# Performance work log

Hardware: AMD Instinct MI355X
Metric: run time of the kernel (lower is better)

Reference implementation:

```python
import jax, jax.numpy as jnp
import numpy as np
import math

B, N0 = 128, 128          # graphs, nodes per graph
EPG = 512                 # edges per graph
F_IN, EDGE_DIM = 64, 16
EMB, HEADS = 128, 4
HC = EMB * HEADS
L = 2                     # stacked layers (pooling every layer: top_k_every_n=1)
RATIO = 0.5
DENSE = 256


def setup_inputs():
    rng = np.random.default_rng(0)

    def U(fan_in, *shape):
        s = 1.0 / np.sqrt(fan_in)
        return jnp.asarray(rng.uniform(-s, s, shape), dtype=jnp.float32)

    x = jnp.asarray(rng.standard_normal((B * N0, F_IN)), dtype=jnp.float32)
    src = rng.integers(0, N0, (B, EPG))
    dst = rng.integers(0, N0, (B, EPG))
    off = (np.arange(B) * N0)[:, None]
    edge_index = jnp.asarray(np.stack([(src + off).reshape(-1), (dst + off).reshape(-1)]), dtype=jnp.int32)
    edge_attr = jnp.asarray(rng.standard_normal((B * EPG, EDGE_DIM)), dtype=jnp.float32)

    inp = dict(x=x, edge_index=edge_index, edge_attr=edge_attr)
    inp.update(
        c1_Wq=U(F_IN, F_IN, HC), c1_bq=U(F_IN, HC),
        c1_Wk=U(F_IN, F_IN, HC), c1_bk=U(F_IN, HC),
        c1_Wv=U(F_IN, F_IN, HC), c1_bv=U(F_IN, HC),
        c1_We=U(EDGE_DIM, EDGE_DIM, HC),
        c1_Ws=U(F_IN, F_IN, HC), c1_bs=U(F_IN, HC),
        c1_Wb=U(3 * HC, 3 * HC),
        t1_W=U(HC, HC, EMB), t1_b=U(HC, EMB),
        bn1_g=jnp.ones(EMB), bn1_b=jnp.zeros(EMB),
        cl_Wq=U(EMB, L, EMB, HC), cl_bq=U(EMB, L, HC),
        cl_Wk=U(EMB, L, EMB, HC), cl_bk=U(EMB, L, HC),
        cl_Wv=U(EMB, L, EMB, HC), cl_bv=U(EMB, L, HC),
        cl_We=U(EDGE_DIM, L, EDGE_DIM, HC),
        cl_Ws=U(EMB, L, EMB, HC), cl_bs=U(EMB, L, HC),
        cl_Wb=U(3 * HC, L, 3 * HC),
        tl_W=U(HC, L, HC, EMB), tl_b=U(HC, L, EMB),
        bnl_g=jnp.ones((L, EMB)), bnl_b=jnp.zeros((L, EMB)),
        pool_w=U(EMB, L, EMB),
        l1_W=U(2 * EMB, 2 * EMB, DENSE), l1_b=U(2 * EMB, DENSE),
        l2_W=U(DENSE, DENSE, DENSE // 2), l2_b=U(DENSE, DENSE // 2),
        l3_W=U(DENSE // 2, DENSE // 2, 1), l3_b=U(DENSE // 2, 1),
    )
    return inp


def _tconv(x, src, dst, emask, ea, Wq, bq, Wk, bk, Wv, bv, We, Ws, bs, Wb, n_nodes):
    # PyG TransformerConv, beta=True, concat=True, edge features added to key and value
    H, C = HEADS, EMB
    q = (x @ Wq + bq).reshape(-1, H, C)
    k = (x @ Wk + bk).reshape(-1, H, C)
    v = (x @ Wv + bv).reshape(-1, H, C)
    e = (ea @ We).reshape(-1, H, C)
    kj = k[src] + e
    alpha = (q[dst] * kj).sum(-1) * (1.0 / math.sqrt(C))  # [E, H]
    mx = jax.ops.segment_max(jnp.where(emask[:, None], alpha, -jnp.inf), dst, num_segments=n_nodes)
    mx = jnp.where(jnp.isfinite(mx), mx, 0.0)
    p = jnp.where(emask[:, None], jnp.exp(alpha - mx[dst]), 0.0)
    p = p / (jax.ops.segment_sum(p, dst, num_segments=n_nodes)[dst] + 1e-16)
    msg = v[src] + e
    out = jax.ops.segment_sum(p[:, :, None] * msg, dst, num_segments=n_nodes).reshape(-1, H * C)
    skip = x @ Ws + bs
    beta = jax.nn.sigmoid(jnp.concatenate([out, skip, out - skip], -1) @ Wb)[:, None]
    return beta * skip + (1.0 - beta) * out


def _bn(x, g, b):
    # BatchNorm1d, training-mode batch statistics (biased variance)
    m = x.mean(0)
    v = ((x - m) ** 2).mean(0)
    return g * (x - m) * jax.lax.rsqrt(v + 1e-5) + b


def _topk_pool(x, src, dst, emask, w, n):
    # TopKPooling: score = x.w/|w|, keep top ceil(ratio*n) per graph, scale by tanh(score)
    k = int(math.ceil(RATIO * n))
    s = (x @ w) / jnp.linalg.norm(w)          # [B*n]
    _, idx = jax.lax.top_k(s.reshape(B, n), k)
    idx = jnp.sort(idx, axis=1)
    gidx = (jnp.arange(B)[:, None] * n + idx).reshape(-1)
    x_new = x[gidx] * jnp.tanh(s[gidx])[:, None]
    kept = jnp.zeros(B * n, bool).at[gidx].set(True)
    new_id = (jnp.cumsum(kept) - 1).astype(jnp.int32)
    em = emask & kept[src] & kept[dst]
    src_n = jnp.where(em, new_id[src], 0)
    dst_n = jnp.where(em, new_id[dst], 0)
    return x_new, src_n, dst_n, em, k


def _forward(edge_index, x, edge_attr, c1_Wq, c1_bq, c1_Wk, c1_bk, c1_Wv, c1_bv, c1_We, c1_Ws, c1_bs, c1_Wb,
             t1_W, t1_b, bn1_g, bn1_b, cl_Wq, cl_bq, cl_Wk, cl_bk, cl_Wv, cl_bv, cl_We, cl_Ws, cl_bs, cl_Wb,
             tl_W, tl_b, bnl_g, bnl_b, pool_w, l1_W, l1_b, l2_W, l2_b, l3_W, l3_b):
    src, dst = edge_index[0], edge_index[1]
    emask = jnp.ones(src.shape[0], bool)
    n = N0
    x = _tconv(x, src, dst, emask, edge_attr, c1_Wq, c1_bq, c1_Wk, c1_bk, c1_Wv, c1_bv, c1_We, c1_Ws, c1_bs, c1_Wb, B * n)
    x = _bn(jax.nn.relu(x @ t1_W + t1_b), bn1_g, bn1_b)
    reps = []
    for i in range(L):
        x = _tconv(x, src, dst, emask, edge_attr, cl_Wq[i], cl_bq[i], cl_Wk[i], cl_bk[i], cl_Wv[i], cl_bv[i],
                   cl_We[i], cl_Ws[i], cl_bs[i], cl_Wb[i], B * n)
        x = _bn(jax.nn.relu(x @ tl_W[i] + tl_b[i]), bnl_g[i], bnl_b[i])
        x, src, dst, emask, n = _topk_pool(x, src, dst, emask, pool_w[i], n)
        xg = x.reshape(B, n, EMB)
        reps.append(jnp.concatenate([xg.max(1), xg.mean(1)], -1))  # gmp || gap
    h = reps[0]
    for r in reps[1:]:
        h = h + r
    h = jax.nn.relu(h @ l1_W + l1_b)  # dropout p=0.8 is identity at eval
    h = jax.nn.relu(h @ l2_W + l2_b)
    return h @ l3_W + l3_b            # [B, 1]


def reference(x, edge_index, edge_attr, c1_Wq, c1_bq, c1_Wk, c1_bk, c1_Wv, c1_bv, c1_We, c1_Ws, c1_bs, c1_Wb,
              t1_W, t1_b, bn1_g, bn1_b, cl_Wq, cl_bq, cl_Wk, cl_bk, cl_Wv, cl_bv, cl_We, cl_Ws, cl_bs, cl_Wb,
              tl_W, tl_b, bnl_g, bnl_b, pool_w, l1_W, l1_b, l2_W, l2_b, l3_W, l3_b):
    return _forward(edge_index, x, edge_attr, c1_Wq, c1_bq, c1_Wk, c1_bk, c1_Wv, c1_bv, c1_We, c1_Ws, c1_bs, c1_Wb,
                    t1_W, t1_b, bn1_g, bn1_b, cl_Wq, cl_bq, cl_Wk, cl_bk, cl_Wv, cl_bv, cl_We, cl_Ws, cl_bs, cl_Wb,
                    tl_W, tl_b, bnl_g, bnl_b, pool_w, l1_W, l1_b, l2_W, l2_b, l3_W, l3_b)
```

## Files before the change

kernel.cpp:

```cpp
#include <hip/hip_runtime.h>
#include <math.h>

#define E_TOT 65536
#define B_G   128
#define QLD   1664
#define NCOL  1792

typedef __attribute__((ext_vector_type(8))) short short8;
typedef __attribute__((ext_vector_type(4))) short short4v;
typedef __attribute__((ext_vector_type(4))) float float4v;

__device__ __forceinline__ unsigned short f2bf(float f) {
    unsigned int u = __float_as_uint(f);
    unsigned int r = u + 0x7FFFu + ((u >> 16) & 1u);
    return (unsigned short)(r >> 16);
}
__device__ __forceinline__ float bf2f(unsigned short h) {
    return __uint_as_float(((unsigned int)h) << 16);
}

__global__ void wsplit_k(const float* __restrict__ Wst, const float* __restrict__ Wq,
                         const float* __restrict__ Wk, const float* __restrict__ Wvt,
                         const float* __restrict__ Wu, const float* __restrict__ Wvz,
                         const float* __restrict__ ws_z,
                         int K, int kshift, unsigned short* __restrict__ Whi,
                         unsigned short* __restrict__ Wlo) {
    int idx = blockIdx.x * 256 + threadIdx.x;
    if (idx >= NCOL * K) return;
    int col = idx >> kshift, k = idx & (K - 1);
    float w;
    if (col < 128)       w = Wst[k * 128 + col];
    else if (col < 640)  w = Wq[(size_t)k * 512 + col - 128];
    else if (col < 1152) w = Wk[(size_t)k * 512 + col - 640];
    else if (col < 1664) w = Wvt[(size_t)k * 512 + col - 1152];
    else if (col < 1728) w = Wu[(size_t)k * 64 + col - 1664];
    else if (col < 1732) w = Wvz[(size_t)k * 4 + col - 1728];
    else if (col == 1732) w = ws_z[k];
    else                 w = 0.f;
    unsigned short h = f2bf(w);
    Whi[idx] = h;
    Wlo[idx] = f2bf(w - bf2f(h));
}

__global__ void xsplit_k(const float* __restrict__ X, int total4,
                         unsigned short* __restrict__ Xhi, unsigned short* __restrict__ Xlo) {
    int idx = blockIdx.x * 256 + threadIdx.x;
    if (idx >= total4) return;
    float4 f = ((const float4*)X)[idx];
    unsigned short h0 = f2bf(f.x), h1 = f2bf(f.y), h2 = f2bf(f.z), h3 = f2bf(f.w);
    short4v hv = {(short)h0, (short)h1, (short)h2, (short)h3};
    short4v lv = {(short)f2bf(f.x - bf2f(h0)), (short)f2bf(f.y - bf2f(h1)),
                  (short)f2bf(f.z - bf2f(h2)), (short)f2bf(f.w - bf2f(h3))};
    *(short4v*)(Xhi + (size_t)idx * 4) = hv;
    *(short4v*)(Xlo + (size_t)idx * 4) = lv;
}

__global__ void twt_k(const float* __restrict__ tW, float* __restrict__ tWT) {
    int idx = blockIdx.x * 256 + threadIdx.x;
    int m = idx & 127, c = idx >> 7;
    tWT[m * 512 + c] = tW[idx];
}

template <int KT>
__global__ __launch_bounds__(256) void qkvs_mfma(
        const unsigned short* __restrict__ Xhi, const unsigned short* __restrict__ Xlo,
        const unsigned short* __restrict__ Whi, const unsigned short* __restrict__ Wlo,
        const float* __restrict__ bq, const float* __restrict__ bk,
        const float* __restrict__ bvt, const float* __restrict__ bu,
        const float* __restrict__ bvz, const float* __restrict__ zb,
        float* __restrict__ out, float* __restrict__ UB, float* __restrict__ VZB,
        float* __restrict__ SZB, int nwg8) {
    constexpr int NKC = KT >> 5;
    constexpr int NCH = KT >> 6;
    __shared__ __align__(16) unsigned short bs[2 * 64 * 80];
    const int ldb = 80, loHalf = 64 * 80;
    int tid = threadIdx.x;
    int wave = tid >> 6, lane = tid & 63;
    int m = lane & 15, kg = lane >> 4;
    int hw = blockIdx.y * 28 + blockIdx.x;
    int lb = (hw & 7) * nwg8 + (hw >> 3);
    int n0 = (lb / 28) * 128 + wave * 32;
    int c0 = (lb % 28) * 64;

    short8 ahi[2][NKC], alo[2][NKC];
#pragma unroll
    for (int rt = 0; rt < 2; ++rt) {
        const unsigned short* xh = Xhi + (size_t)(n0 + rt * 16 + m) * KT + kg * 8;
        const unsigned short* xl = Xlo + (size_t)(n0 + rt * 16 + m) * KT + kg * 8;
#pragma unroll
        for (int kc = 0; kc < NKC; ++kc) {
            ahi[rt][kc] = *(const short8*)(xh + kc * 32);
            alo[rt][kc] = *(const short8*)(xl + kc * 32);
        }
    }

    float4v acc[2][4];
#pragma unroll
    for (int rt = 0; rt < 2; ++rt)
#pragma unroll
        for (int ct = 0; ct < 4; ++ct) acc[rt][ct] = (float4v){0.f, 0.f, 0.f, 0.f};

    short8 ph[2][2], pl[2][2];
#pragma unroll
    for (int it = 0; it < 2; ++it) {
        int i = tid + it * 256; int col = i >> 3, part = i & 7;
        ph[0][it] = *(const short8*)(Whi + (size_t)(c0 + col) * KT + part * 8);
        pl[0][it] = *(const short8*)(Wlo + (size_t)(c0 + col) * KT + part * 8);
    }

#pragma unroll
    for (int ch = 0; ch < NCH; ++ch) {
        if (ch) __syncthreads();
#pragma unroll
        for (int it = 0; it < 2; ++it) {
            int i = tid + it * 256; int col = i >> 3, part = i & 7;
            *(short8*)(bs + col * ldb + part * 8) = ph[ch & 1][it];
            *(short8*)(bs + loHalf + col * ldb + part * 8) = pl[ch & 1][it];
        }
        __syncthreads();
        if (ch + 1 < NCH) {
#pragma unroll
            for (int it = 0; it < 2; ++it) {
                int i = tid + it * 256; int col = i >> 3, part = i & 7;
                ph[(ch + 1) & 1][it] =
                    *(const short8*)(Whi + (size_t)(c0 + col) * KT + (ch + 1) * 64 + part * 8);
                pl[(ch + 1) & 1][it] =
                    *(const short8*)(Wlo + (size_t)(c0 + col) * KT + (ch + 1) * 64 + part * 8);
            }
        }
#pragma unroll
        for (int kc2 = 0; kc2 < 2; ++kc2) {
            const int kc = ch * 2 + kc2;
#pragma unroll
            for (int ct = 0; ct < 4; ++ct) {
                const unsigned short* bp = bs + (ct * 16 + m) * ldb + kg * 8 + kc2 * 32;
                short8 bhi = *(const short8*)(bp);
                short8 blo = *(const short8*)(bp + loHalf);
                acc[0][ct] = __builtin_amdgcn_mfma_f32_16x16x32_bf16(ahi[0][kc], bhi, acc[0][ct], 0, 0, 0);
                acc[0][ct] = __builtin_amdgcn_mfma_f32_16x16x32_bf16(alo[0][kc], bhi, acc[0][ct], 0, 0, 0);
                acc[0][ct] = __builtin_amdgcn_mfma_f32_16x16x32_bf16(ahi[0][kc], blo, acc[0][ct], 0, 0, 0);
                acc[1][ct] = __builtin_amdgcn_mfma_f32_16x16x32_bf16(ahi[1][kc], bhi, acc[1][ct], 0, 0, 0);
                acc[1][ct] = __builtin_amdgcn_mfma_f32_16x16x32_bf16(alo[1][kc], bhi, acc[1][ct], 0, 0, 0);
                acc[1][ct] = __builtin_amdgcn_mfma_f32_16x16x32_bf16(ahi[1][kc], blo, acc[1][ct], 0, 0, 0);
            }
        }
    }

#pragma unroll
    for (int ct = 0; ct < 4; ++ct) {
        int col = c0 + ct * 16 + m;
        if (col > 1732) continue;
        float bias;
        if (col < 128)       bias = 0.f;
        else if (col < 640)  bias = bq[col - 128];
        else if (col < 1152) bias = bk[col - 640];
        else if (col < 1664) bias = bvt[col - 1152];
        else if (col < 1728) bias = bu[col - 1664];
        else if (col < 1732) bias = bvz[col - 1728];
        else                 bias = zb[0];
#pragma unroll
        for (int rt = 0; rt < 2; ++rt) {
#pragma unroll
            for (int r = 0; r < 4; ++r) {
                int row = n0 + rt * 16 + kg * 4 + r;
                float v = acc[rt][ct][r] + bias;
                if (col < 1664)      out[(size_t)row * QLD + col] = v;
                else if (col < 1728) UB[(size_t)row * 64 + col - 1664] = v;
                else if (col < 1732) VZB[(size_t)row * 4 + col - 1728] = v;
                else                 SZB[row] = v;
            }
        }
    }
}

__global__ void prep_k(const float* __restrict__ Ws, const float* __restrict__ bs,
                       const float* __restrict__ tWT, const float* __restrict__ Wb,
                       const float* __restrict__ Wq, const float* __restrict__ bq,
                       const float* __restrict__ We,
                       const float* __restrict__ Wv, const float* __restrict__ bv, int Fin,
                       float* __restrict__ Wst, float* __restrict__ ws_z,
                       float* __restrict__ sbt, float* __restrict__ zb,
                       float* __restrict__ Wu, float* __restrict__ bu,
                       float* __restrict__ Wet, float* __restrict__ wez,
                       float* __restrict__ Wvt, float* __restrict__ bvt,
                       float* __restrict__ Wvz, float* __restrict__ bvz) {
    int w = (blockIdx.x * blockDim.x + threadIdx.x) >> 6;
    int lane = threadIdx.x & 63;
    int o1 = Fin * 128, o2 = o1 + Fin, o3 = o2 + 128, o4 = o3 + 1;
    int o5 = o4 + Fin * 64, o6 = o5 + 64, o7 = o6 + 8192, o8 = o7 + 64;
    int o9 = o8 + Fin * 512, o10 = o9 + 512, o11 = o10 + Fin * 4, total = o11 + 4;
    if (w >= total) return;
    float s = 0.f;
    if (w < o1) {
        int f = w >> 7, m = w & 127;
        for (int c = lane; c < 512; c += 64)
            s = fmaf(Ws[(size_t)f * 512 + c], tWT[(size_t)m * 512 + c], s);
    } else if (w < o2) {
        int f = w - o1;
        for (int c = lane; c < 512; c += 64)
            s = fmaf(Ws[(size_t)f * 512 + c], Wb[512 + c] - Wb[1024 + c], s);
    } else if (w < o3) {
        int m = w - o2;
        for (int c = lane; c < 512; c += 64)
            s = fmaf(bs[c], tWT[(size_t)m * 512 + c], s);
    } else if (w < o4) {
        for (int c = lane; c < 512; c += 64)
            s = fmaf(bs[c], Wb[512 + c] - Wb[1024 + c], s);
    } else if (w < o5) {
        int q = w - o4; int f = q >> 6; int j2 = q & 63;
        int j = j2 & 15; int cb = (j2 >> 4) * 128;
        s = Wq[(size_t)f * 512 + cb + lane] * We[j * 512 + cb + lane]
          + Wq[(size_t)f * 512 + cb + lane + 64] * We[j * 512 + cb + lane + 64];
    } else if (w < o6) {
        int j2 = w - o5; int j = j2 & 15; int cb = (j2 >> 4) * 128;
        s = bq[cb + lane] * We[j * 512 + cb + lane]
          + bq[cb + lane + 64] * We[j * 512 + cb + lane + 64];
    } else if (w < o7) {
        int q = w - o6; int j2 = q >> 7; int m = q & 127;
        int j = j2 & 15; int cb = (j2 >> 4) * 128;
        s = We[j * 512 + cb + lane] * tWT[(size_t)m * 512 + cb + lane]
          + We[j * 512 + cb + lane + 64] * tWT[(size_t)m * 512 + cb + lane + 64];
    } else if (w < o8) {
        int j2 = w - o7; int j = j2 & 15; int cb = (j2 >> 4) * 128;
        s = We[j * 512 + cb + lane] * (Wb[cb + lane] + Wb[1024 + cb + lane])
          + We[j * 512 + cb + lane + 64] * (Wb[cb + lane + 64] + Wb[1024 + cb + lane + 64]);
    } else if (w < o9) {
        int q = w - o8; int f = q >> 9; int j2 = q & 511;
        int cb = (j2 >> 7) * 128; int m = j2 & 127;
        s = Wv[(size_t)f * 512 + cb + lane] * tWT[(size_t)m * 512 + cb + lane]
          + Wv[(size_t)f * 512 + cb + lane + 64] * tWT[(size_t)m * 512 + cb + lane + 64];
    } else if (w < o10) {
        int j2 = w - o9; int cb = (j2 >> 7) * 128; int m = j2 & 127;
        s = bv[cb + lane] * tWT[(size_t)m * 512 + cb + lane]
          + bv[cb + lane + 64] * tWT[(size_t)m * 512 + cb + lane + 64];
    } else if (w < o11) {
        int q = w - o10; int f = q >> 2; int cb = (q & 3) * 128;
        s = Wv[(size_t)f * 512 + cb + lane] * (Wb[cb + lane] + Wb[1024 + cb + lane])
          + Wv[(size_t)f * 512 + cb + lane + 64] * (Wb[cb + lane + 64] + Wb[1024 + cb + lane + 64]);
    } else {
        int cb = (w - o11) * 128;
        s = bv[cb + lane] * (Wb[cb + lane] + Wb[1024 + cb + lane])
          + bv[cb + lane + 64] * (Wb[cb + lane + 64] + Wb[1024 + cb + lane + 64]);
    }
#pragma unroll
    for (int off = 32; off; off >>= 1) s += __shfl_xor(s, off, 64);
    if (lane == 0) {
        if (w < o1) Wst[w] = s;
        else if (w < o2) ws_z[w - o1] = s;
        else if (w < o3) sbt[w - o2] = s;
        else if (w < o4) zb[0] = s;
        else if (w < o5) Wu[w - o4] = s;
        else if (w < o6) bu[w - o5] = s;
        else if (w < o7) Wet[w - o6] = s;
        else if (w < o8) wez[w - o7] = s;
        else if (w < o9) Wvt[w - o8] = s;
        else if (w < o10) bvt[w - o9] = s;
        else if (w < o11) Wvz[w - o10] = s;
        else bvz[w - o11] = s;
    }
}

__global__ __launch_bounds__(128) void csr_graph_k(const int* __restrict__ src,
                                                   const int* __restrict__ dst,
                                                   int* __restrict__ row_start,
                                                   int* __restrict__ row_end,
                                                   int* __restrict__ colb,
                                                   int* __restrict__ eidb) {
    __shared__ int cnt[128], pref[128], cur[128];
    int g = blockIdx.x, t = threadIdx.x;
    cnt[t] = 0;
    __syncthreads();
    int e0 = g * 512, nb = g * 128;
    int dl[4], sl[4];
#pragma unroll
    for (int i = 0; i < 4; ++i) {
        int e = e0 + t + i * 128;
        dl[i] = dst[e] - nb;
        sl[i] = src[e];
        atomicAdd(&cnt[dl[i]], 1);
    }
    __syncthreads();
    pref[t] = cnt[t];
    __syncthreads();
    for (int st = 1; st < 128; st <<= 1) {
        int v = (t >= st) ? pref[t - st] : 0;
        __syncthreads();
        pref[t] += v;
        __syncthreads();
    }
    int ex = pref[t] - cnt[t];
    row_start[nb + t] = e0 + ex;
    row_end[nb + t]   = e0 + pref[t];
    cur[t] = ex;
    __syncthreads();
#pragma unroll
    for (int i = 0; i < 4; ++i) {
        int pos = atomicAdd(&cur[dl[i]], 1);
        colb[e0 + pos] = sl[i];
        eidb[e0 + pos] = e0 + t + i * 128;
    }
}

__global__ __launch_bounds__(256) void attn_combine_k(
        const float* __restrict__ QB, const float* __restrict__ UB,
        const float* __restrict__ VZB, const float* __restrict__ SZB,
        const int* __restrict__ row_start, const int* __restrict__ row_end,
        const int* __restrict__ colb, const int* __restrict__ eidb,
        const float* __restrict__ ea, const float* __restrict__ wez,
        const float* __restrict__ Wet, const float* __restrict__ sbt,
        const float* __restrict__ tb, float* __restrict__ xn, int nwg8) {
    __shared__ float shO[4][4][128];
    __shared__ float tsh[4][64];
    __shared__ float zsh[4][4];
    int tid = threadIdx.x;
    int head = tid >> 6, lane = tid & 63;
    int grp = lane >> 4, li = lane & 15;
    int bid = blockIdx.x;
    int lb = (bid & 7) * nwg8 + (bid >> 3);
    int node = lb * 4 + grp;

    float wezv = wez[head * 16 + li];
    const float* Qr = QB + (size_t)node * QLD + 128 + head * 128 + li * 8;
    float4 q0 = *(const float4*)Qr;
    float4 q1 = *(const float4*)(Qr + 4);
    float uu = UB[(size_t)node * 64 + head * 16 + li];
    int beg = row_start[node], end = row_end[node];

    float l = 0.f, t = 0.f, zac = 0.f;
    float4 a0 = {0.f, 0.f, 0.f, 0.f}, a1 = {0.f, 0.f, 0.f, 0.f};
    const float scale = 0.08838834764831845f;
    int j = beg;
    for (; j + 1 < end; j += 2) {
        int s1 = colb[j],     e1 = eidb[j];
        int s2 = colb[j + 1], e2 = eidb[j + 1];
        const float* K1 = QB + (size_t)s1 * QLD + 640 + head * 128 + li * 8;
        const float* V1 = QB + (size_t)s1 * QLD + 1152 + head * 128 + li * 8;
        const float* K2 = QB + (size_t)s2 * QLD + 640 + head * 128 + li * 8;
        const float* V2 = QB + (size_t)s2 * QLD + 1152 + head * 128 + li * 8;
        float4 k10 = *(const float4*)K1, k11 = *(const float4*)(K1 + 4);
        float4 v10 = *(const float4*)V1, v11 = *(const float4*)(V1 + 4);
        float4 k20 = *(const float4*)K2, k21 = *(const float4*)(K2 + 4);
// ... 258 lines not shown
                       const float* __restrict__ W3, const float* __restrict__ b3,
                       float* __restrict__ out) {
    __shared__ float h[256], a1[256], a2[128], red[256];
    int g = blockIdx.x, t = threadIdx.x;
    h[t] = rep0[g * 256 + t] + rep1[g * 256 + t];
    __syncthreads();
    float acc = b1[t];
    for (int i = 0; i < 256; ++i) acc = fmaf(h[i], W1[i * 256 + t], acc);
    a1[t] = fmaxf(acc, 0.f);
    __syncthreads();
    if (t < 128) {
        float a = b2[t];
        for (int i = 0; i < 256; ++i) a = fmaf(a1[i], W2[i * 128 + t], a);
        a2[t] = fmaxf(a, 0.f);
    }
    __syncthreads();
    red[t] = (t < 128) ? a2[t] * W3[t] : 0.f;
    __syncthreads();
    for (int st = 128; st; st >>= 1) {
        if (t < st) red[t] += red[t + st];
        __syncthreads();
    }
    if (t == 0) out[g] = red[0] + b3[0];
}

extern "C" void kernel_launch(void* const* d_in, const int* in_sizes, int n_in,
                              void* d_out, int out_size, void* d_ws, size_t ws_size,
                              hipStream_t stream) {
    (void)in_sizes; (void)n_in; (void)out_size; (void)ws_size;

    const float* x0    = (const float*)d_in[0];
    const int*   ei    = (const int*)d_in[1];
    const float* ea    = (const float*)d_in[2];
    const float* c1_Wq = (const float*)d_in[3];
    const float* c1_bq = (const float*)d_in[4];
    const float* c1_Wk = (const float*)d_in[5];
    const float* c1_bk = (const float*)d_in[6];
    const float* c1_Wv = (const float*)d_in[7];
    const float* c1_bv = (const float*)d_in[8];
    const float* c1_We = (const float*)d_in[9];
    const float* c1_Ws = (const float*)d_in[10];
    const float* c1_bs = (const float*)d_in[11];
    const float* c1_Wb = (const float*)d_in[12];
    const float* t1_W  = (const float*)d_in[13];
    const float* t1_b  = (const float*)d_in[14];
    const float* bn1_g = (const float*)d_in[15];
    const float* bn1_b = (const float*)d_in[16];
    const float* cl_Wq = (const float*)d_in[17];
    const float* cl_bq = (const float*)d_in[18];
    const float* cl_Wk = (const float*)d_in[19];
    const float* cl_bk = (const float*)d_in[20];
    const float* cl_Wv = (const float*)d_in[21];
    const float* cl_bv = (const float*)d_in[22];
    const float* cl_We = (const float*)d_in[23];
    const float* cl_Ws = (const float*)d_in[24];
    const float* cl_bs = (const float*)d_in[25];
    const float* cl_Wb = (const float*)d_in[26];
    const float* tl_W  = (const float*)d_in[27];
    const float* tl_b  = (const float*)d_in[28];
    const float* bnl_g = (const float*)d_in[29];
    const float* bnl_b = (const float*)d_in[30];
    const float* pool_w= (const float*)d_in[31];
    const float* l1_W  = (const float*)d_in[32];
    const float* l1_b  = (const float*)d_in[33];
    const float* l2_W  = (const float*)d_in[34];
    const float* l2_b  = (const float*)d_in[35];
    const float* l3_W  = (const float*)d_in[36];
    const float* l3_b  = (const float*)d_in[37];
    float* out = (float*)d_out;

    char* base = (char*)d_ws;
    size_t off = 0;
    auto alloc = [&](size_t bytes) -> void* {
        void* p = base + off;
        off += (bytes + 255) & ~(size_t)255;
        return p;
    };
    float* QB   = (float*)alloc((size_t)16384 * QLD * 4);
    float* xA   = (float*)alloc((size_t)16384 * 128 * 4);
    float* xB   = (float*)alloc((size_t)16384 * 128 * 4);
    float* UB   = (float*)alloc((size_t)16384 * 64 * 4);
    float* VZB  = (float*)alloc((size_t)16384 * 4 * 4);
    float* SZB  = (float*)alloc((size_t)16384 * 4);
    float* Wst  = (float*)alloc(128 * 128 * 4);
    float* ws_z = (float*)alloc(128 * 4);
    float* sbt  = (float*)alloc(128 * 4);
    float* zb   = (float*)alloc(4 * 4);
    float* Wu   = (float*)alloc(128 * 64 * 4);
    float* bu   = (float*)alloc(64 * 4);
    float* Wet  = (float*)alloc(64 * 128 * 4);
    float* wez  = (float*)alloc(64 * 4);
    float* Wvt  = (float*)alloc(128 * 512 * 4);
    float* bvt  = (float*)alloc(512 * 4);
    float* Wvz  = (float*)alloc(128 * 4 * 4);
    float* bvz  = (float*)alloc(4 * 4);
    float* tWT  = (float*)alloc(128 * 512 * 4);
    float* stats  = (float*)alloc(256 * 4);
    float* scores = (float*)alloc(16384 * 4);
    float* rep0   = (float*)alloc(128 * 256 * 4);
    float* rep1   = (float*)alloc(128 * 256 * 4);
    int* row_start = (int*)alloc(16384 * 4);
    int* row_end   = (int*)alloc(16384 * 4);
    int* colb      = (int*)alloc(E_TOT * 4);
    int* eidb      = (int*)alloc(E_TOT * 4);
    unsigned short* Whi = (unsigned short*)alloc((size_t)NCOL * 128 * 2);
    unsigned short* Wlo = (unsigned short*)alloc((size_t)NCOL * 128 * 2);
    unsigned short* Xhi = (unsigned short*)alloc((size_t)16384 * 128 * 2);
    unsigned short* Xlo = (unsigned short*)alloc((size_t)16384 * 128 * 2);
    float* xp = xA;

    auto tconv = [&](int N, int Fin,
                     const float* Wq, const float* bq, const float* Wk, const float* bk,
                     const float* Wv, const float* bv, const float* We,
                     const float* Ws, const float* bs, const float* Wb,
                     const float* tW, const float* tb, float* xn) {
        int total = Fin * 128 + Fin + 129 + Fin * 64 + 64 + 8192 + 64
                  + Fin * 512 + 512 + Fin * 4 + 4;
        twt_k<<<256, 256, 0, stream>>>(tW, tWT);
        prep_k<<<(total + 3) / 4, 256, 0, stream>>>(Ws, bs, tWT, Wb, Wq, bq, We, Wv, bv, Fin,
                                                    Wst, ws_z, sbt, zb, Wu, bu, Wet, wez,
                                                    Wvt, bvt, Wvz, bvz);
        int kshift = (Fin == 64) ? 6 : 7;
        wsplit_k<<<(NCOL * Fin + 255) / 256, 256, 0, stream>>>(Wst, Wq, Wk, Wvt, Wu, Wvz,
                                                               ws_z, Fin, kshift, Whi, Wlo);
        int nwg8 = 28 * (N / 128) / 8;
        if (Fin == 64)
            qkvs_mfma<64><<<dim3(28, N / 128), 256, 0, stream>>>(Xhi, Xlo, Whi, Wlo,
                                                                 bq, bk, bvt, bu, bvz, zb,
                                                                 QB, UB, VZB, SZB, nwg8);
        else
            qkvs_mfma<128><<<dim3(28, N / 128), 256, 0, stream>>>(Xhi, Xlo, Whi, Wlo,
                                                                  bq, bk, bvt, bu, bvz, zb,
                                                                  QB, UB, VZB, SZB, nwg8);
        attn_combine_k<<<N / 4, 256, 0, stream>>>(QB, UB, VZB, SZB,
                                                  row_start, row_end, colb, eidb,
                                                  ea, wez, Wet, sbt, tb, xn, N / 32);
    };

    csr_graph_k<<<B_G, 128, 0, stream>>>(ei, ei + E_TOT, row_start, row_end, colb, eidb);

    xsplit_k<<<(16384 * 64 / 4 + 255) / 256, 256, 0, stream>>>(x0, 16384 * 64 / 4, Xhi, Xlo);
    tconv(16384, 64, c1_Wq, c1_bq, c1_Wk, c1_bk, c1_Wv, c1_bv, c1_We,
          c1_Ws, c1_bs, c1_Wb, t1_W, t1_b, xA);
    hipMemsetAsync(stats, 0, 256 * 4, stream);
    bn_stats_k<<<512, 128, 0, stream>>>(xA, 16384, stats);
    bn_apply_k<<<(16384 * 128 + 255) / 256, 256, 0, stream>>>(xA, 16384, stats, bn1_g, bn1_b,
                                                              Xhi, Xlo);

    tconv(16384, 128, cl_Wq, cl_bq, cl_Wk, cl_bk, cl_Wv, cl_bv, cl_We,
          cl_Ws, cl_bs, cl_Wb, tl_W, tl_b, xB);
    hipMemsetAsync(stats, 0, 256 * 4, stream);
    bn_stats_k<<<512, 128, 0, stream>>>(xB, 16384, stats);
    bn_apply_score_k<<<16384 / 4, 256, 0, stream>>>(xB, 16384, stats, bnl_g, bnl_b,
                                                    pool_w, scores);

    topk_pool0_k<<<B_G, 128, 0, stream>>>(scores, xB, ei, ei + E_TOT, xp, rep0,
                                          row_start, row_end, colb, eidb, Xhi, Xlo);

    tconv(8192, 128,
          cl_Wq + 65536, cl_bq + 512, cl_Wk + 65536, cl_bk + 512,
          cl_Wv + 65536, cl_bv + 512, cl_We + 8192,
          cl_Ws + 65536, cl_bs + 512, cl_Wb + 1536,
          tl_W + 65536, tl_b + 128, xB);
    hipMemsetAsync(stats, 0, 256 * 4, stream);
    bn_stats_k<<<512, 128, 0, stream>>>(xB, 8192, stats);
    bn_apply_score_k<<<8192 / 4, 256, 0, stream>>>(xB, 8192, stats, bnl_g + 128, bnl_b + 128,
                                                   pool_w + 128, scores);

    topk_pool1_k<<<B_G, 128, 0, stream>>>(scores, xB, rep1);

    head_k<<<B_G, 256, 0, stream>>>(rep0, rep1, l1_W, l1_b, l2_W, l2_b, l3_W, l3_b, out);
}
```

Baseline: 538.8 us.

## Batch weight prep for all layers into single launches; double rows per GEMM block

Weight preprocessing (transpose, prep, bf16 hi/lo split) for all three TransformerConv layers is now done up front in three launches using a blockIdx.y layer selector, replacing nine per-layer launches. Each layer gets its own buffers. The QKVS MFMA kernel now stages the whole weight panel in LDS once and processes two 128-row groups per block, halving the grid and reusing the B tile. The cost is more LDS per block, which may reduce occupancy, and fewer blocks in flight.

```diff
diff --git a/kernel.cpp b/kernel.cpp
--- a/kernel.cpp
+++ b/kernel.cpp
@@ -19,177 +19,38 @@
     return __uint_as_float(((unsigned int)h) << 16);
 }
 
-__global__ void wsplit_k(const float* __restrict__ Wst, const float* __restrict__ Wq,
-                         const float* __restrict__ Wk, const float* __restrict__ Wvt,
-                         const float* __restrict__ Wu, const float* __restrict__ Wvz,
-                         const float* __restrict__ ws_z,
-                         int K, int kshift, unsigned short* __restrict__ Whi,
-                         unsigned short* __restrict__ Wlo) {
-    int idx = blockIdx.x * 256 + threadIdx.x;
-    if (idx >= NCOL * K) return;
-    int col = idx >> kshift, k = idx & (K - 1);
-    float w;
-    if (col < 128)       w = Wst[k * 128 + col];
-    else if (col < 640)  w = Wq[(size_t)k * 512 + col - 128];
-    else if (col < 1152) w = Wk[(size_t)k * 512 + col - 640];
-    else if (col < 1664) w = Wvt[(size_t)k * 512 + col - 1152];
-    else if (col < 1728) w = Wu[(size_t)k * 64 + col - 1664];
-    else if (col < 1732) w = Wvz[(size_t)k * 4 + col - 1728];
-    else if (col == 1732) w = ws_z[k];
-    else                 w = 0.f;
-    unsigned short h = f2bf(w);
-    Whi[idx] = h;
-    Wlo[idx] = f2bf(w - bf2f(h));
-}
-
-__global__ void xsplit_k(const float* __restrict__ X, int total4,
-                         unsigned short* __restrict__ Xhi, unsigned short* __restrict__ Xlo) {
-    int idx = blockIdx.x * 256 + threadIdx.x;
-    if (idx >= total4) return;
-    float4 f = ((const float4*)X)[idx];
-    unsigned short h0 = f2bf(f.x), h1 = f2bf(f.y), h2 = f2bf(f.z), h3 = f2bf(f.w);
-    short4v hv = {(short)h0, (short)h1, (short)h2, (short)h3};
-    short4v lv = {(short)f2bf(f.x - bf2f(h0)), (short)f2bf(f.y - bf2f(h1)),
-                  (short)f2bf(f.z - bf2f(h2)), (short)f2bf(f.w - bf2f(h3))};
-    *(short4v*)(Xhi + (size_t)idx * 4) = hv;
-    *(short4v*)(Xlo + (size_t)idx * 4) = lv;
-}
-
-__global__ void twt_k(const float* __restrict__ tW, float* __restrict__ tWT) {
+struct LayerPrep {
+    const float *Ws, *bs_, *Wq, *bq, *We, *Wv, *bv, *tW;
+    float *Wst, *ws_z, *sbt, *zb, *Wu, *bu, *Wet, *wez, *Wvt, *bvt, *Wvz, *bvz, *tWT;
+    unsigned short *Whi, *Wlo;
+    int Fin;
+};
+
+__device__ __forceinline__ LayerPrep pick(const LayerPrep& p0, const LayerPrep& p1,
+                                          const LayerPrep& p2) {
+    return blockIdx.y == 0 ? p0 : (blockIdx.y == 1 ? p1 : p2);
+}
+
+__global__ void twt_all_k(LayerPrep p0, LayerPrep p1, LayerPrep p2) {
+    LayerPrep p = pick(p0, p1, p2);
     int idx = blockIdx.x * 256 + threadIdx.x;
     int m = idx & 127, c = idx >> 7;
-    tWT[m * 512 + c] = tW[idx];
-}
-
-template <int KT>
-__global__ __launch_bounds__(256) void qkvs_mfma(
-        const unsigned short* __restrict__ Xhi, const unsigned short* __restrict__ Xlo,
-        const unsigned short* __restrict__ Whi, const unsigned short* __restrict__ Wlo,
-        const float* __restrict__ bq, const float* __restrict__ bk,
-        const float* __restrict__ bvt, const float* __restrict__ bu,
-        const float* __restrict__ bvz, const float* __restrict__ zb,
-        float* __restrict__ out, float* __restrict__ UB, float* __restrict__ VZB,
-        float* __restrict__ SZB, int nwg8) {
-    constexpr int NKC = KT >> 5;
-    constexpr int NCH = KT >> 6;
-    __shared__ __align__(16) unsigned short bs[2 * 64 * 80];
-    const int ldb = 80, loHalf = 64 * 80;
-    int tid = threadIdx.x;
-    int wave = tid >> 6, lane = tid & 63;
-    int m = lane & 15, kg = lane >> 4;
-    int hw = blockIdx.y * 28 + blockIdx.x;
-    int lb = (hw & 7) * nwg8 + (hw >> 3);
-    int n0 = (lb / 28) * 128 + wave * 32;
-    int c0 = (lb % 28) * 64;
-
-    short8 ahi[2][NKC], alo[2][NKC];
-#pragma unroll
-    for (int rt = 0; rt < 2; ++rt) {
-        const unsigned short* xh = Xhi + (size_t)(n0 + rt * 16 + m) * KT + kg * 8;
-        const unsigned short* xl = Xlo + (size_t)(n0 + rt * 16 + m) * KT + kg * 8;
-#pragma unroll
-        for (int kc = 0; kc < NKC; ++kc) {
-            ahi[rt][kc] = *(const short8*)(xh + kc * 32);
-            alo[rt][kc] = *(const short8*)(xl + kc * 32);
-        }
-    }
-
-    float4v acc[2][4];
-#pragma unroll
-    for (int rt = 0; rt < 2; ++rt)
-#pragma unroll
-        for (int ct = 0; ct < 4; ++ct) acc[rt][ct] = (float4v){0.f, 0.f, 0.f, 0.f};
-
-    short8 ph[2][2], pl[2][2];
-#pragma unroll
-    for (int it = 0; it < 2; ++it) {
-        int i = tid + it * 256; int col = i >> 3, part = i & 7;
-        ph[0][it] = *(const short8*)(Whi + (size_t)(c0 + col) * KT + part * 8);
-        pl[0][it] = *(const short8*)(Wlo + (size_t)(c0 + col) * KT + part * 8);
-    }
-
-#pragma unroll
-    for (int ch = 0; ch < NCH; ++ch) {
-        if (ch) __syncthreads();
-#pragma unroll
-        for (int it = 0; it < 2; ++it) {
-            int i = tid + it * 256; int col = i >> 3, part = i & 7;
-            *(short8*)(bs + col * ldb + part * 8) = ph[ch & 1][it];
-            *(short8*)(bs + loHalf + col * ldb + part * 8) = pl[ch & 1][it];
-        }
-        __syncthreads();
-        if (ch + 1 < NCH) {
-#pragma unroll
-            for (int it = 0; it < 2; ++it) {
-                int i = tid + it * 256; int col = i >> 3, part = i & 7;
-                ph[(ch + 1) & 1][it] =
-                    *(const short8*)(Whi + (size_t)(c0 + col) * KT + (ch + 1) * 64 + part * 8);
-                pl[(ch + 1) & 1][it] =
-                    *(const short8*)(Wlo + (size_t)(c0 + col) * KT + (ch + 1) * 64 + part * 8);
-            }
-        }
-#pragma unroll
-        for (int kc2 = 0; kc2 < 2; ++kc2) {
-            const int kc = ch * 2 + kc2;
-#pragma unroll
-            for (int ct = 0; ct < 4; ++ct) {
-                const unsigned short* bp = bs + (ct * 16 + m) * ldb + kg * 8 + kc2 * 32;
-                short8 bhi = *(const short8*)(bp);
-                short8 blo = *(const short8*)(bp + loHalf);
-                acc[0][ct] = __builtin_amdgcn_mfma_f32_16x16x32_bf16(ahi[0][kc], bhi, acc[0][ct], 0, 0, 0);
-                acc[0][ct] = __builtin_amdgcn_mfma_f32_16x16x32_bf16(alo[0][kc], bhi, acc[0][ct], 0, 0, 0);
-                acc[0][ct] = __builtin_amdgcn_mfma_f32_16x16x32_bf16(ahi[0][kc], blo, acc[0][ct], 0, 0, 0);
-                acc[1][ct] = __builtin_amdgcn_mfma_f32_16x16x32_bf16(ahi[1][kc], bhi, acc[1][ct], 0, 0, 0);
-                acc[1][ct] = __builtin_amdgcn_mfma_f32_16x16x32_bf16(alo[1][kc], bhi, acc[1][ct], 0, 0, 0);
-                acc[1][ct] = __builtin_amdgcn_mfma_f32_16x16x32_bf16(ahi[1][kc], blo, acc[1][ct], 0, 0, 0);
-            }
-        }
-    }
-
-#pragma unroll
-    for (int ct = 0; ct < 4; ++ct) {
-        int col = c0 + ct * 16 + m;
-        if (col > 1732) continue;
-        float bias;
-        if (col < 128)       bias = 0.f;
-        else if (col < 640)  bias = bq[col - 128];
-        else if (col < 1152) bias = bk[col - 640];
-        else if (col < 1664) bias = bvt[col - 1152];
-        else if (col < 1728) bias = bu[col - 1664];
-        else if (col < 1732) bias = bvz[col - 1728];
-        else                 bias = zb[0];
-#pragma unroll
-        for (int rt = 0; rt < 2; ++rt) {
-#pragma unroll
-            for (int r = 0; r < 4; ++r) {
-                int row = n0 + rt * 16 + kg * 4 + r;
-                float v = acc[rt][ct][r] + bias;
-                if (col < 1664)      out[(size_t)row * QLD + col] = v;
-                else if (col < 1728) UB[(size_t)row * 64 + col - 1664] = v;
-                else if (col < 1732) VZB[(size_t)row * 4 + col - 1728] = v;
-                else                 SZB[row] = v;
-            }
-        }
-    }
-}
-
-__global__ void prep_k(const float* __restrict__ Ws, const float* __restrict__ bs,
-                       const float* __restrict__ tWT, const float* __restrict__ Wb,
-                       const float* __restrict__ Wq, const float* __restrict__ bq,
-                       const float* __restrict__ We,
-                       const float* __restrict__ Wv, const float* __restrict__ bv, int Fin,
-                       float* __restrict__ Wst, float* __restrict__ ws_z,
-                       float* __restrict__ sbt, float* __restrict__ zb,
-                       float* __restrict__ Wu, float* __restrict__ bu,
-                       float* __restrict__ Wet, float* __restrict__ wez,
-                       float* __restrict__ Wvt, float* __restrict__ bvt,
-                       float* __restrict__ Wvz, float* __restrict__ bvz) {
+    p.tWT[m * 512 + c] = p.tW[idx];
+}
+
+__global__ void prep_all_k(LayerPrep p0, LayerPrep p1, LayerPrep p2, const float* Wb0,
+                           const float* Wb1, const float* Wb2) {
+    LayerPrep p = pick(p0, p1, p2);
+    const float* Wb = blockIdx.y == 0 ? Wb0 : (blockIdx.y == 1 ? Wb1 : Wb2);
+    int Fin = p.Fin;
     int w = (blockIdx.x * blockDim.x + threadIdx.x) >> 6;
     int lane = threadIdx.x & 63;
     int o1 = Fin * 128, o2 = o1 + Fin, o3 = o2 + 128, o4 = o3 + 1;
     int o5 = o4 + Fin * 64, o6 = o5 + 64, o7 = o6 + 8192, o8 = o7 + 64;
     int o9 = o8 + Fin * 512, o10 = o9 + 512, o11 = o10 + Fin * 4, total = o11 + 4;
     if (w >= total) return;
+    const float *Ws = p.Ws, *bs = p.bs_, *tWT = p.tWT, *Wq = p.Wq, *bq = p.bq,
+                *We = p.We, *Wv = p.Wv, *bv = p.bv;
     float s = 0.f;
     if (w < o1) {
         int f = w >> 7, m = w & 127;
@@ -245,18 +106,168 @@
 #pragma unroll
     for (int off = 32; off; off >>= 1) s += __shfl_xor(s, off, 64);
     if (lane == 0) {
-        if (w < o1) Wst[w] = s;
-        else if (w < o2) ws_z[w - o1] = s;
-        else if (w < o3) sbt[w - o2] = s;
-        else if (w < o4) zb[0] = s;
-        else if (w < o5) Wu[w - o4] = s;
-        else if (w < o6) bu[w - o5] = s;
-        else if (w < o7) Wet[w - o6] = s;
-        else if (w < o8) wez[w - o7] = s;
-        else if (w < o9) Wvt[w - o8] = s;
-        else if (w < o10) bvt[w - o9] = s;
-        else if (w < o11) Wvz[w - o10] = s;
-        else bvz[w - o11] = s;
+        if (w < o1) p.Wst[w] = s;
+        else if (w < o2) p.ws_z[w - o1] = s;
+        else if (w < o3) p.sbt[w - o2] = s;
+        else if (w < o4) p.zb[0] = s;
+        else if (w < o5) p.Wu[w - o4] = s;
+        else if (w < o6) p.bu[w - o5] = s;
+        else if (w < o7) p.Wet[w - o6] = s;
+        else if (w < o8) p.wez[w - o7] = s;
+        else if (w < o9) p.Wvt[w - o8] = s;
+        else if (w < o10) p.bvt[w - o9] = s;
+        else if (w < o11) p.Wvz[w - o10] = s;
+        else p.bvz[w - o11] = s;
+    }
+}
+
+__global__ void wsplit_all_k(LayerPrep p0, LayerPrep p1, LayerPrep p2,
+                             const float* Wk0, const float* Wk1, const float* Wk2) {
+    LayerPrep p = pick(p0, p1, p2);
+    const float* Wk = blockIdx.y == 0 ? Wk0 : (blockIdx.y == 1 ? Wk1 : Wk2);
+    int K = p.Fin, kshift = (K == 64) ? 6 : 7;
+    int idx = blockIdx.x * 256 + threadIdx.x;
+    if (idx >= NCOL * K) return;
+    int col = idx >> kshift, k = idx & (K - 1);
+    float w;
+    if (col < 128)       w = p.Wst[k * 128 + col];
+    else if (col < 640)  w = p.Wq[(size_t)k * 512 + col - 128];
+    else if (col < 1152) w = Wk[(size_t)k * 512 + col - 640];
+    else if (col < 1664) w = p.Wvt[(size_t)k * 512 + col - 1152];
+    else if (col < 1728) w = p.Wu[(size_t)k * 64 + col - 1664];
+    else if (col < 1732) w = p.Wvz[(size_t)k * 4 + col - 1728];
+    else if (col == 1732) w = p.ws_z[k];
+    else                 w = 0.f;
+    unsigned short h = f2bf(w);
+    p.Whi[idx] = h;
+    p.Wlo[idx] = f2bf(w - bf2f(h));
+}
+
+__global__ void xsplit_k(const float* __restrict__ X, int total4,
+                         unsigned short* __restrict__ Xhi, unsigned short* __restrict__ Xlo) {
+    int idx = blockIdx.x * 256 + threadIdx.x;
+    if (idx >= total4) return;
+    float4 f = ((const float4*)X)[idx];
+    unsigned short h0 = f2bf(f.x), h1 = f2bf(f.y), h2 = f2bf(f.z), h3 = f2bf(f.w);
+    short4v hv = {(short)h0, (short)h1, (short)h2, (short)h3};
+    short4v lv = {(short)f2bf(f.x - bf2f(h0)), (short)f2bf(f.y - bf2f(h1)),
+                  (short)f2bf(f.z - bf2f(h2)), (short)f2bf(f.w - bf2f(h3))};
+    *(short4v*)(Xhi + (size_t)idx * 4) = hv;
+    *(short4v*)(Xlo + (size_t)idx * 4) = lv;
+}
+
+template <int KT>
+__global__ __launch_bounds__(256) void qkvs_mfma(
+        const unsigned short* __restrict__ Xhi, const unsigned short* __restrict__ Xlo,
+        const unsigned short* __restrict__ Whi, const unsigned short* __restrict__ Wlo,
+        const float* __restrict__ bq, const float* __restrict__ bk,
+        const float* __restrict__ bvt, const float* __restrict__ bu,
+        const float* __restrict__ bvz, const float* __restrict__ zb,
+        float* __restrict__ out, float* __restrict__ UB, float* __restrict__ VZB,
+        float* __restrict__ SZB, int nwg8) {
+    constexpr int NKC = KT >> 5;
+    constexpr int NCH = KT >> 6;
+    __shared__ __align__(16) unsigned short bs[NCH * 2 * 64 * 80];
+    const int ldb = 80;
+    int tid = threadIdx.x;
+    int wave = tid >> 6, lane = tid & 63;
+    int m = lane & 15, kg = lane >> 4;
+    int hw = blockIdx.y * 28 + blockIdx.x;
+    int lb = (hw & 7) * nwg8 + (hw >> 3);
+    int rb = (lb / 28) * 256;
+    int c0 = (lb % 28) * 64;
+
+    short8 ahi[2][NKC], alo[2][NKC];
+    auto loadA = [&](int n0) {
+#pragma unroll
+        for (int rt = 0; rt < 2; ++rt) {
+            const unsigned short* xh = Xhi + (size_t)(n0 + rt * 16 + m) * KT + kg * 8;
+            const unsigned short* xl = Xlo + (size_t)(n0 + rt * 16 + m) * KT + kg * 8;
+#pragma unroll
+            for (int kc = 0; kc < NKC; ++kc) {
+                ahi[rt][kc] = *(const short8*)(xh + kc * 32);
+                alo[rt][kc] = *(const short8*)(xl + kc * 32);
+            }
+        }
+    };
+    loadA(rb + wave * 32);
+
+    for (int i = tid; i < NCH * 64 * 8; i += 256) {
+        int ch = i >> 9;
+        int r = i & 511; int col = r >> 3, part = r & 7;
+        unsigned short* dst = bs + ch * (2 * 64 * 80);
+        *(short8*)(dst + col * ldb + part * 8) =
+            *(const short8*)(Whi + (size_t)(c0 + col) * KT + ch * 64 + part * 8);
+        *(short8*)(dst + 64 * 80 + col * ldb + part * 8) =
+            *(const short8*)(Wlo + (size_t)(c0 + col) * KT + ch * 64 + part * 8);
+    }
+    __syncthreads();
+
+    float bias[4];
+#pragma unroll
+    for (int ct = 0; ct < 4; ++ct) {
+        int col = c0 + ct * 16 + m;
+        float bv_;
+        if (col < 128)       bv_ = 0.f;
+        else if (col < 640)  bv_ = bq[col - 128];
+        else if (col < 1152) bv_ = bk[col - 640];
+        else if (col < 1664) bv_ = bvt[col - 1152];
+        else if (col < 1728) bv_ = bu[col - 1664];
+        else if (col < 1732) bv_ = bvz[col - 1728];
+        else if (col == 1732) bv_ = zb[0];
+        else                 bv_ = 0.f;
+        bias[ct] = bv_;
+    }
+
+#pragma unroll
+    for (int rg = 0; rg < 2; ++rg) {
+        int n0 = rb + rg * 128 + wave * 32;
+        if (rg) loadA(n0);
+
+        float4v acc[2][4];
+#pragma unroll
+        for (int rt = 0; rt < 2; ++rt)
+#pragma unroll
+            for (int ct = 0; ct < 4; ++ct) acc[rt][ct] = (float4v){0.f, 0.f, 0.f, 0.f};
+
+#pragma unroll
+        for (int ch = 0; ch < NCH; ++ch) {
+            const unsigned short* bsc = bs + ch * (2 * 64 * 80);
+#pragma unroll
+            for (int kc2 = 0; kc2 < 2; ++kc2) {
+                const int kc = ch * 2 + kc2;
+#pragma unroll
+                for (int ct = 0; ct < 4; ++ct) {
+                    const unsigned short* bp = bsc + (ct * 16 + m) * ldb + kg * 8 + kc2 * 32;
+                    short8 bhi = *(const short8*)(bp);
+                    short8 blo = *(const short8*)(bp + 64 * 80);
+                    acc[0][ct] = __builtin_amdgcn_mfma_f32_16x16x32_bf16(ahi[0][kc], bhi, acc[0][ct], 0, 0, 0);
+                    acc[0][ct] = __builtin_amdgcn_mfma_f32_16x16x32_bf16(alo[0][kc], bhi, acc[0][ct], 0, 0, 0);
+                    acc[0][ct] = __builtin_amdgcn_mfma_f32_16x16x32_bf16(ahi[0][kc], blo, acc[0][ct], 0, 0, 0);
+                    acc[1][ct] = __builtin_amdgcn_mfma_f32_16x16x32_bf16(ahi[1][kc], bhi, acc[1][ct], 0, 0, 0);
+                    acc[1][ct] = __builtin_amdgcn_mfma_f32_16x16x32_bf16(alo[1][kc], bhi, acc[1][ct], 0, 0, 0);
+                    acc[1][ct] = __builtin_amdgcn_mfma_f32_16x16x32_bf16(ahi[1][kc], blo, acc[1][ct], 0, 0, 0);
+                }
+            }
+        }
+
+#pragma unroll
+        for (int ct = 0; ct < 4; ++ct) {
+            int col = c0 + ct * 16 + m;
+            if (col > 1732) continue;
+#pragma unroll
+            for (int rt = 0; rt < 2; ++rt) {
+#pragma unroll
+                for (int r = 0; r < 4; ++r) {
+                    int row = n0 + rt * 16 + kg * 4 + r;
+                    float v = acc[rt][ct][r] + bias[ct];
+                    if (col < 1664)      out[(size_t)row * QLD + col] = v;
+                    else if (col < 1728) UB[(size_t)row * 64 + col - 1664] = v;
+                    else if (col < 1732) VZB[(size_t)row * 4 + col - 1728] = v;
+                    else                 SZB[row] = v;
+                }
+            }
+        }
     }
 }
 
@@ -681,19 +692,6 @@
     float* UB   = (float*)alloc((size_t)16384 * 64 * 4);
     float* VZB  = (float*)alloc((size_t)16384 * 4 * 4);
     float* SZB  = (float*)alloc((size_t)16384 * 4);
-    float* Wst  = (float*)alloc(128 * 128 * 4);
-    float* ws_z = (float*)alloc(128 * 4);
-    float* sbt  = (float*)alloc(128 * 4);
-    float* zb   = (float*)alloc(4 * 4);
-    float* Wu   = (float*)alloc(128 * 64 * 4);
-    float* bu   = (float*)alloc(64 * 4);
-    float* Wet  = (float*)alloc(64 * 128 * 4);
-    float* wez  = (float*)alloc(64 * 4);
-    float* Wvt  = (float*)alloc(128 * 512 * 4);
-    float* bvt  = (float*)alloc(512 * 4);
-    float* Wvz  = (float*)alloc(128 * 4 * 4);
-    float* bvz  = (float*)alloc(4 * 4);
-    float* tWT  = (float*)alloc(128 * 512 * 4);
     float* stats  = (float*)alloc(256 * 4);
     float* scores = (float*)alloc(16384 * 4);
     float* rep0   = (float*)alloc(128 * 256 * 4);
@@ -702,52 +700,79 @@
     int* row_end   = (int*)alloc(16384 * 4);
     int* colb      = (int*)alloc(E_TOT * 4);
     int* eidb      = (int*)alloc(E_TOT * 4);
-    unsigned short* Whi = (unsigned short*)alloc((size_t)NCOL * 128 * 2);
-    unsigned short* Wlo = (unsigned short*)alloc((size_t)NCOL * 128 * 2);
     unsigned short* Xhi = (unsigned short*)alloc((size_t)16384 * 128 * 2);
     unsigned short* Xlo = (unsigned short*)alloc((size_t)16384 * 128 * 2);
+
+    LayerPrep P[3];
+    const float* Wb_[3] = {c1_Wb, cl_Wb, cl_Wb + 1536};
+    const float* Wk_[3] = {c1_Wk, cl_Wk, cl_Wk + 65536};
+    for (int l = 0; l < 3; ++l) {
+        LayerPrep& p = P[l];
+        p.Wst  = (float*)alloc(128 * 128 * 4);
+        p.ws_z = (float*)alloc(128 * 4);
+        p.sbt  = (float*)alloc(128 * 4);
+        p.zb   = (float*)alloc(16);
+        p.Wu   = (float*)alloc(128 * 64 * 4);
+        p.bu   = (float*)alloc(64 * 4);
+        p.Wet  = (float*)alloc(64 * 128 * 4);
+        p.wez  = (float*)alloc(64 * 4);
+        p.Wvt  = (float*)alloc(128 * 512 * 4);
+        p.bvt  = (float*)alloc(512 * 4);
+        p.Wvz  = (float*)alloc(128 * 4 * 4);
+        p.bvz  = (float*)alloc(16);
+        p.tWT  = (float*)alloc(128 * 512 * 4);
+        p.Whi  = (unsigned short*)alloc((size_t)NCOL * 128 * 2);
+        p.Wlo  = (unsigned short*)alloc((size_t)NCOL * 128 * 2);
+    }
+    P[0].Ws = c1_Ws; P[0].bs_ = c1_bs; P[0].Wq = c1_Wq; P[0].bq = c1_bq;
+    P[0].We = c1_We; P[0].Wv = c1_Wv; P[0].bv = c1_bv; P[0].tW = t1_W; P[0].Fin = 64;
+    P[1].Ws = cl_Ws; P[1].bs_ = cl_bs; P[1].Wq = cl_Wq; P[1].bq = cl_bq;
+    P[1].We = cl_We; P[1].Wv = cl_Wv; P[1].bv = cl_bv; P[1].tW = tl_W; P[1].Fin = 128;
+    P[2].Ws = cl_Ws + 65536; P[2].bs_ = cl_bs + 512; P[2].Wq = cl_Wq + 65536;
+    P[2].bq = cl_bq + 512; P[2].We = cl_We + 8192; P[2].Wv = cl_Wv + 65536;
+    P[2].bv = cl_bv + 512; P[2].tW = tl_W + 65536; P[2].Fin = 128;
+
     float* xp = xA;
 
-    auto tconv = [&](int N, int Fin,
-                     const float* Wq, const float* bq, const float* Wk, const float* bk,
-                     const float* Wv, const float* bv, const float* We,
-                     const float* Ws, const float* bs, const float* Wb,
-                     const float* tW, const float* tb, float* xn) {
-        int total = Fin * 128 + Fin + 129 + Fin * 64 + 64 + 8192 + 64
-                  + Fin * 512 + 512 + Fin * 4 + 4;
-        twt_k<<<256, 256, 0, stream>>>(tW, tWT);
-        prep_k<<<(total + 3) / 4, 256, 0, stream>>>(Ws, bs, tWT, Wb, Wq, bq, We, Wv, bv, Fin,
-                                                    Wst, ws_z, sbt, zb, Wu, bu, Wet, wez,
-                                                    Wvt, bvt, Wvz, bvz);
-        int kshift = (Fin == 64) ? 6 : 7;
-        wsplit_k<<<(NCOL * Fin + 255) / 256, 256, 0, stream>>>(Wst, Wq, Wk, Wvt, Wu, Wvz,
-                                                               ws_z, Fin, kshift, Whi, Wlo);
-        int nwg8 = 28 * (N / 128) / 8;
-        if (Fin == 64)
-            qkvs_mfma<64><<<dim3(28, N / 128), 256, 0, stream>>>(Xhi, Xlo, Whi, Wlo,
-                                                                 bq, bk, bvt, bu, bvz, zb,
+    twt_all_k<<<dim3(256, 3), 256, 0, stream>>>(P[0], P[1], P[2]);
+    {
+        int totalMax = 128 * 128 + 128 + 129 + 128 * 64 + 64 + 8192 + 64
+                     + 128 * 512 + 512 + 128 * 4 + 4;
+        prep_all_k<<<dim3((totalMax + 3) / 4, 3), 256, 0, stream>>>(P[0], P[1], P[2],
+                                                                    Wb_[0], Wb_[1], Wb_[2]);
+        wsplit_all_k<<<dim3((NCOL * 128 + 255) / 256, 3), 256, 0, stream>>>(P[0], P[1], P[2],
+                                                                            Wk_[0], Wk_[1], Wk_[2]);
+    }
+
+    csr_graph_k<<<B_G, 128, 0, stream>>>(ei, ei + E_TOT, row_start, row_end, colb, eidb);
+    xsplit_k<<<(16384 * 64 / 4 + 255) / 256, 256, 0, stream>>>(x0, 16384 * 64 / 4, Xhi, Xlo);
+
+    auto tconv = [&](int L, int N, const float* bq, const float* bk, const float* tb,
+                     float* xn) {
+        int nwg8 = 28 * (N / 256) / 8;
+        if (P[L].Fin == 64)
+            qkvs_mfma<64><<<dim3(28, N / 256), 256, 0, stream>>>(Xhi, Xlo, P[L].Whi, P[L].Wlo,
+                                                                 bq, bk, P[L].bvt, P[L].bu,
+                                                                 P[L].bvz, P[L].zb,
                                                                  QB, UB, VZB, SZB, nwg8);
         else
-            qkvs_mfma<128><<<dim3(28, N / 128), 256, 0, stream>>>(Xhi, Xlo, Whi, Wlo,
-                                                                  bq, bk, bvt, bu, bvz, zb,
+            qkvs_mfma<128><<<dim3(28, N / 256), 256, 0, stream>>>(Xhi, Xlo, P[L].Whi, P[L].Wlo,
+                                                                  bq, bk, P[L].bvt, P[L].bu,
+                                                                  P[L].bvz, P[L].zb,
                                                                   QB, UB, VZB, SZB, nwg8);
         attn_combine_k<<<N / 4, 256, 0, stream>>>(QB, UB, VZB, SZB,
                                                   row_start, row_end, colb, eidb,
-                                                  ea, wez, Wet, sbt, tb, xn, N / 32);
+                                                  ea, P[L].wez, P[L].Wet, P[L].sbt, tb,
+                                                  xn, N / 32);
     };
 
-    csr_graph_k<<<B_G, 128, 0, stream>>>(ei, ei + E_TOT, row_start, row_end, colb, eidb);
-
-    xsplit_k<<<(16384 * 64 / 4 + 255) / 256, 256, 0, stream>>>(x0, 16384 * 64 / 4, Xhi, Xlo);
-    tconv(16384, 64, c1_Wq, c1_bq, c1_Wk, c1_bk, c1_Wv, c1_bv, c1_We,
-          c1_Ws, c1_bs, c1_Wb, t1_W, t1_b, xA);
+    tconv(0, 16384, c1_bq, c1_bk, t1_b, xA);
     hipMemsetAsync(stats, 0, 256 * 4, stream);
     bn_stats_k<<<512, 128, 0, stream>>>(xA, 16384, stats);
     bn_apply_k<<<(16384 * 128 + 255) / 256, 256, 0, stream>>>(xA, 16384, stats, bn1_g, bn1_b,
                                                               Xhi, Xlo);
 
-    tconv(16384, 128, cl_Wq, cl_bq, cl_Wk, cl_bk, cl_Wv, cl_bv, cl_We,
-          cl_Ws, cl_bs, cl_Wb, tl_W, tl_b, xB);
+    tconv(1, 16384, cl_bq, cl_bk, tl_b, xB);
     hipMemsetAsync(stats, 0, 256 * 4, stream);
     bn_stats_k<<<512, 128, 0, stream>>>(xB, 16384, stats);
     bn_apply_score_k<<<16384 / 4, 256, 0, stream>>>(xB, 16384, stats, bnl_g, bnl_b,
@@ -756,11 +781,7 @@
     topk_pool0_k<<<B_G, 128, 0, stream>>>(scores, xB, ei, ei + E_TOT, xp, rep0,
                                           row_start, row_end, colb, eidb, Xhi, Xlo);
 
-    tconv(8192, 128,
-          cl_Wq + 65536, cl_bq + 512, cl_Wk + 65536, cl_bk + 512,
-          cl_Wv + 65536, cl_bv + 512, cl_We + 8192,
-          cl_Ws + 65536, cl_bs + 512, cl_Wb + 1536,
-          tl_W + 65536, tl_b + 128, xB);
+    tconv(2, 8192, cl_bq + 512, cl_bk + 512, tl_b + 128, xB);
     hipMemsetAsync(stats, 0, 256 * 4, stream);
     bn_stats_k<<<512, 128, 0, stream>>>(xB, 8192, stats);
     bn_apply_score_k<<<8192 / 4, 256, 0, stream>>>(xB, 8192, stats, bnl_g + 128, bnl_b + 128,
```

Result: slower. 570.8 us (+5.9%).
